# Kernel tuning notes

Hardware: AMD Instinct MI355X
Metric: run time of the kernel (lower is better)

The kernel has to match this reference:

```python
import jax, jax.numpy as jnp
import numpy as np

NUM_HEADS = 8
NUM_GROUPS = 32
EPS = 1e-5


def group_norm(x, gamma, beta):
    B, C, H, W = x.shape
    xg = x.reshape(B, NUM_GROUPS, C // NUM_GROUPS * H * W)
    mean = xg.mean(axis=-1, keepdims=True)
    var = xg.var(axis=-1, keepdims=True)
    xg = (xg - mean) * jax.lax.rsqrt(var + EPS)
    xn = xg.reshape(B, C, H, W)
    return xn * gamma[None, :, None, None] + beta[None, :, None, None]


def setup_inputs() -> dict:
    key = jax.random.key(0)
    ks = jax.random.split(key, 7)
    C = 512
    B, H, W = 8, 32, 32
    x = jax.random.normal(ks[0], (B, C, H, W), dtype=jnp.float32)
    gamma = jnp.ones((C,), dtype=jnp.float32)
    beta = jnp.zeros((C,), dtype=jnp.float32)
    # 1x1 conv weights stored as [out, in]
    w_qkv = jax.random.normal(ks[1], (3 * C, C), dtype=jnp.float32) * (1.0 / np.sqrt(C))
    b_qkv = jax.random.normal(ks[2], (3 * C,), dtype=jnp.float32) * 0.02
    w_proj = jax.random.normal(ks[3], (C, C), dtype=jnp.float32) * (1.0 / np.sqrt(C))
    b_proj = jax.random.normal(ks[4], (C,), dtype=jnp.float32) * 0.02
    return {"x": x, "gamma": gamma, "beta": beta, "w_qkv": w_qkv,
            "b_qkv": b_qkv, "w_proj": w_proj, "b_proj": b_proj}


def reference(x, gamma, beta, w_qkv, b_qkv, w_proj, b_proj):
    B, C, H, W = x.shape
    hd = C // NUM_HEADS  # head_dim
    x_norm = group_norm(x, gamma, beta)
    # 1x1 conv: [B,C,H,W] x [3C,C] -> [B,3C,H,W]
    qkv = jnp.einsum('bchw,oc->bohw', x_norm, w_qkv) + b_qkv[None, :, None, None]
    q, k, v = jnp.split(qkv, 3, axis=1)
    N = H * W
    q = q.reshape(B, NUM_HEADS, hd, N)
    k = k.reshape(B, NUM_HEADS, hd, N)
    v = v.reshape(B, NUM_HEADS, hd, N)
    attn = jnp.einsum('bhcn,bhcm->bhnm', q, k) * (hd ** -0.5)
    attn = jax.nn.softmax(attn, axis=-1)
    out = jnp.einsum('bhnm,bhcm->bhcn', attn, v)
    out = out.reshape(B, C, H, W)
    proj = jnp.einsum('bchw,oc->bohw', out, w_proj) + b_proj[None, :, None, None]
    return x + proj
```

## Files before the change

kernel.cpp:

```cpp
#include <hip/hip_runtime.h>
#include <hip/hip_bf16.h>

#define BB 8
#define CC 512
#define NN 1024
#define NG 32
#define CPG 16
#define NH 8
#define HD 64
#define C3 1536
#define QKLD 1024

typedef __hip_bfloat16 bf16;
typedef unsigned short ushort_t;

typedef __attribute__((ext_vector_type(8))) short bf16x8;
typedef __attribute__((ext_vector_type(8))) unsigned short ushortx8;
typedef __attribute__((ext_vector_type(4))) float floatx4;

__device__ __forceinline__ float b2f(bf16 h) { return __bfloat162float(h); }
__device__ __forceinline__ bf16 f2b(float f) { return __float2bfloat16(f); }
__device__ __forceinline__ float us2f(ushort_t u) {
    union { unsigned int i; float f; } c; c.i = ((unsigned int)u) << 16; return c.f;
}
__device__ __forceinline__ ushort_t f2us(float f) {
    bf16 h = __float2bfloat16(f);
    return *(ushort_t*)&h;
}

__global__ __launch_bounds__(256) void gn_kernel(const float* __restrict__ x,
                                                 const float* __restrict__ gamma,
                                                 const float* __restrict__ beta,
                                                 bf16* __restrict__ xnT,
                                                 const float* __restrict__ wqkv,
                                                 const float* __restrict__ wproj,
                                                 ushort_t* __restrict__ wqkvB,
                                                 ushort_t* __restrict__ wprojB) {
    int tid = threadIdx.x;
    if (blockIdx.x >= 256) {
        int wb = blockIdx.x - 256;
        int base = (wb * 256 + tid) * 4;
        const int STR = 16 * 256 * 4;
        for (int i = base; i < C3 * CC; i += STR) {
            float4 f = *(const float4*)(wqkv + i);
            ushort_t u[4] = {f2us(f.x), f2us(f.y), f2us(f.z), f2us(f.w)};
            *(uint2*)(wqkvB + i) = *(uint2*)u;
        }
        for (int i = base; i < CC * CC; i += STR) {
            float4 f = *(const float4*)(wproj + i);
            ushort_t u[4] = {f2us(f.x), f2us(f.y), f2us(f.z), f2us(f.w)};
            *(uint2*)(wprojB + i) = *(uint2*)u;
        }
        return;
    }

    const int GSZ = CPG * NN;
    int b = blockIdx.x >> 5;
    int g = blockIdx.x & 31;
    size_t base = ((size_t)b * CC + (size_t)g * CPG) * NN;

    int c_loc = tid >> 4;
    int nsp   = (tid & 15) * 16;
    const float* srcrow = x + base + (size_t)c_loc * NN;

    float fv[4][16];
    float s = 0.f, s2 = 0.f;
#pragma unroll
    for (int nc = 0; nc < 4; ++nc) {
        int nb = nc * 256 + nsp;
        *(float4*)(fv[nc] + 0)  = *(const float4*)(srcrow + nb + 0);
        *(float4*)(fv[nc] + 4)  = *(const float4*)(srcrow + nb + 4);
        *(float4*)(fv[nc] + 8)  = *(const float4*)(srcrow + nb + 8);
        *(float4*)(fv[nc] + 12) = *(const float4*)(srcrow + nb + 12);
#pragma unroll
        for (int j = 0; j < 16; ++j) { float v = fv[nc][j]; s += v; s2 += v * v; }
    }

#pragma unroll
    for (int off = 32; off > 0; off >>= 1) {
        s  += __shfl_down(s, off, 64);
        s2 += __shfl_down(s2, off, 64);
    }
    __shared__ float rs[4], rs2[4], stat[2];
    __shared__ ushort_t Lt[16][264];
    int wid = tid >> 6, lane = tid & 63;
    if (lane == 0) { rs[wid] = s; rs2[wid] = s2; }
    __syncthreads();
    if (tid == 0) {
        float ts  = rs[0] + rs[1] + rs[2] + rs[3];
        float ts2 = rs2[0] + rs2[1] + rs2[2] + rs2[3];
        float mean = ts * (1.f / GSZ);
        float var  = ts2 * (1.f / GSZ) - mean * mean;
        stat[0] = mean;
        stat[1] = rsqrtf(var + 1e-5f);
    }
    __syncthreads();
    float mean = stat[0], inv = stat[1];

    float ga = gamma[g * CPG + c_loc];
    float be = beta[g * CPG + c_loc];

    for (int nc = 0; nc < 4; ++nc) {
        ushortx8 u0, u1;
#pragma unroll
        for (int j = 0; j < 8; ++j) {
            u0[j] = f2us((fv[nc][j]     - mean) * inv * ga + be);
            u1[j] = f2us((fv[nc][j + 8] - mean) * inv * ga + be);
        }
        *(ushortx8*)&Lt[c_loc][nsp]     = u0;
        *(ushortx8*)&Lt[c_loc][nsp + 8] = u1;
        __syncthreads();
        ushort_t o16[16];
#pragma unroll
        for (int c = 0; c < 16; ++c) o16[c] = Lt[c][tid];
        ushort_t* dst = (ushort_t*)xnT + ((size_t)b * NN + nc * 256 + tid) * CC + g * CPG;
        *(uint4*)dst       = *(const uint4*)(o16);
        *(uint4*)(dst + 8) = *(const uint4*)(o16 + 8);
        __syncthreads();
    }
}

#define GSTR 40
__global__ __launch_bounds__(256) void qkv_gemm(const ushort_t* __restrict__ wB,
                                                const bf16* __restrict__ xnT,
                                                const float* __restrict__ bias,
                                                bf16* __restrict__ qkT,
                                                bf16* __restrict__ vN) {
    __shared__ ushort_t Wl[128 * GSTR];
    __shared__ ushort_t Xl[128 * GSTR];
    int b  = blockIdx.z;
    int o0 = blockIdx.y * 128;
    int n0 = blockIdx.x * 128;
    int tid = threadIdx.x;
    int wv = tid >> 6, ln = tid & 15, qd = (tid >> 4) & 3;
    int wm = wv >> 1, wn = wv & 1;

    int srow = tid >> 1;
    int kh   = (tid & 1) * 16;
    const ushort_t* wp = wB + (size_t)(o0 + srow) * CC + kh;
    const ushort_t* xp = (const ushort_t*)xnT + ((size_t)b * NN + n0 + srow) * CC + kh;

    floatx4 acc[4][4];
#pragma unroll
    for (int i = 0; i < 4; ++i)
#pragma unroll
        for (int j = 0; j < 4; ++j) acc[i][j] = (floatx4){0.f, 0.f, 0.f, 0.f};

    uint4 wr0, wr1, xr0, xr1;
    wr0 = *(const uint4*)(wp);
    wr1 = *(const uint4*)(wp + 8);
    xr0 = *(const uint4*)(xp);
    xr1 = *(const uint4*)(xp + 8);

    for (int k0 = 0; k0 < CC; k0 += 32) {
        *(uint4*)&Wl[srow * GSTR + kh]     = wr0;
        *(uint4*)&Wl[srow * GSTR + kh + 8] = wr1;
        *(uint4*)&Xl[srow * GSTR + kh]     = xr0;
        *(uint4*)&Xl[srow * GSTR + kh + 8] = xr1;
        __syncthreads();
        if (k0 + 32 < CC) {
            int kn = k0 + 32;
            wr0 = *(const uint4*)(wp + kn);
            wr1 = *(const uint4*)(wp + kn + 8);
            xr0 = *(const uint4*)(xp + kn);
            xr1 = *(const uint4*)(xp + kn + 8);
        }
        bf16x8 af[4], bfr[4];
#pragma unroll
        for (int i = 0; i < 4; ++i)
            af[i] = *(const bf16x8*)&Wl[(wm * 64 + i * 16 + ln) * GSTR + qd * 8];
#pragma unroll
        for (int j = 0; j < 4; ++j)
            bfr[j] = *(const bf16x8*)&Xl[(wn * 64 + j * 16 + ln) * GSTR + qd * 8];
#pragma unroll
        for (int i = 0; i < 4; ++i)
#pragma unroll
            for (int j = 0; j < 4; ++j)
                acc[i][j] = __builtin_amdgcn_mfma_f32_16x16x32_bf16(af[i], bfr[j], acc[i][j], 0, 0, 0);
        __syncthreads();
    }

    if (o0 < 1024) {
#pragma unroll
        for (int i = 0; i < 4; ++i) {
            int ob = o0 + wm * 64 + i * 16 + qd * 4;
            float sc = (ob < 512) ? 0.18033688011112042f : 1.0f;
#pragma unroll
            for (int j = 0; j < 4; ++j) {
                int n = n0 + wn * 64 + j * 16 + ln;
                ushort_t pk[4];
#pragma unroll
                for (int r = 0; r < 4; ++r)
                    pk[r] = f2us((acc[i][j][r] + bias[ob + r]) * sc);
                *(uint2*)((ushort_t*)qkT + ((size_t)b * NN + n) * QKLD + ob) = *(uint2*)pk;
            }
        }
    } else {
#pragma unroll
        for (int i = 0; i < 4; ++i) {
#pragma unroll
            for (int r = 0; r < 4; ++r) {
                int o = o0 + wm * 64 + i * 16 + qd * 4 + r;
                float bb = bias[o];
                size_t rb = ((size_t)b * CC + (o - 1024)) * NN + n0 + wn * 64 + ln;
#pragma unroll
                for (int j = 0; j < 4; ++j)
                    vN[rb + j * 16] = f2b(acc[i][j][r] + bb);
            }
        }
    }
}

__global__ __launch_bounds__(256, 4) void attn_kernel(const bf16* __restrict__ qkTp,
                                                      const bf16* __restrict__ vNp,
                                                      bf16* __restrict__ aoT) {
    __shared__ ushort_t Kt[2][64 * 64];
    __shared__ ushort_t Vn[2][64 * 64];
    __shared__ ushort_t Pw[4][16 * 64];

    int h  = blockIdx.x;
    int qt = blockIdx.y;
    int bi = blockIdx.z;
    int q0 = qt * 64;
    int tid = threadIdx.x;
    int wq = tid >> 6;
    int l  = tid & 63;
    int ln = l & 15;
    int qd = (l >> 4) & 3;
    int l7 = ln & 7;
    int lb = ln >> 3;

    const ushort_t* qkT = (const ushort_t*)qkTp;
    const ushort_t* vN  = (const ushort_t*)vNp;

    const ushort_t* qsrc = qkT + ((size_t)bi * NN + q0 + wq * 16 + ln) * QKLD + h * HD + qd * 8;
    bf16x8 aq0 = *(const bf16x8*)(qsrc);
    bf16x8 aq1 = *(const bf16x8*)(qsrc + 32);

    bf16x8 ones;
#pragma unroll
    for (int j = 0; j < 8; ++j) ones[j] = (short)0x3F80;

    floatx4 O[4];
#pragma unroll
    for (int t = 0; t < 4; ++t) O[t] = (floatx4){0.f, 0.f, 0.f, 0.f};
    floatx4 lsum = (floatx4){0.f, 0.f, 0.f, 0.f};

    ushort_t* Pme = &Pw[wq][0];

    int ksl0 = (qd ^ l7) * 8;
    int ksl1 = ((qd + 4) ^ l7) * 8;

    int srow = tid >> 2;
    int g1   = tid & 3;
    int s7   = srow & 7;
    int ko1  = (g1 ^ s7) * 8;
    int ko2  = ((g1 + 4) ^ s7) * 8;
    const ushort_t* ks = qkT + ((size_t)bi * NN + srow) * QKLD + 512 + h * HD + g1 * 8;
    const ushort_t* vs = vN + ((size_t)bi * CC + h * HD + srow) * NN + g1 * 8;

    uint4 kr0 = *(const uint4*)(ks);
    uint4 kr1 = *(const uint4*)(ks + 32);
    uint4 vr0 = *(const uint4*)(vs);
    uint4 vr1 = *(const uint4*)(vs + 32);
    {
        ushort_t* kd = &Kt[0][srow * 64];
        *(uint4*)(kd + ko1) = kr0; *(uint4*)(kd + ko2) = kr1;
        ushort_t* vd = &Vn[0][srow * 64];
        *(uint4*)(vd + ko1) = vr0; *(uint4*)(vd + ko2) = vr1;
    }
    kr0 = *(const uint4*)(ks + (size_t)64 * QKLD);
    kr1 = *(const uint4*)(ks + (size_t)64 * QKLD + 32);
    vr0 = *(const uint4*)(vs + 64);
    vr1 = *(const uint4*)(vs + 64 + 32);
    __syncthreads();

    for (int it = 0; it < 16; ++it) {
        int cur = it & 1;
        const ushort_t* KtC = &Kt[cur][0];
        const ushort_t* VnC = &Vn[cur][0];
        if (it < 15) {
            ushort_t* kd = &Kt[cur ^ 1][srow * 64];
            *(uint4*)(kd + ko1) = kr0; *(uint4*)(kd + ko2) = kr1;
            ushort_t* vd = &Vn[cur ^ 1][srow * 64];
            *(uint4*)(vd + ko1) = vr0; *(uint4*)(vd + ko2) = vr1;
        }
        if (it < 14) {
            size_t mo = (size_t)(it + 2) * 64;
            kr0 = *(const uint4*)(ks + mo * QKLD);
            kr1 = *(const uint4*)(ks + mo * QKLD + 32);
            vr0 = *(const uint4*)(vs + mo);
            vr1 = *(const uint4*)(vs + mo + 32);
        }

        floatx4 S[4];
#pragma unroll
        for (int t = 0; t < 4; ++t) {
            const ushort_t* krow = KtC + (t * 16 + ln) * 64;
            bf16x8 b0 = *(const bf16x8*)(krow + ksl0);
            bf16x8 b1 = *(const bf16x8*)(krow + ksl1);
            floatx4 acc = (floatx4){0.f, 0.f, 0.f, 0.f};
            acc = __builtin_amdgcn_mfma_f32_16x16x32_bf16(aq0, b0, acc, 0, 0, 0);
            acc = __builtin_amdgcn_mfma_f32_16x16x32_bf16(aq1, b1, acc, 0, 0, 0);
            S[t] = acc;
        }

#pragma unroll
        for (int t = 0; t < 4; ++t) {
#pragma unroll
            for (int r = 0; r < 4; ++r) {
                float p = exp2f(S[t][r]);
                int qr = qd * 4 + r;
                Pme[qr * 64 + ((t * 2 + lb) ^ (qr & 7)) * 8 + l7] = f2us(p);
            }
        }
        bf16x8 pa0 = *(const bf16x8*)&Pme[ln * 64 + ksl0];
        bf16x8 pa1 = *(const bf16x8*)&Pme[ln * 64 + ksl1];

        lsum = __builtin_amdgcn_mfma_f32_16x16x32_bf16(pa0, ones, lsum, 0, 0, 0);
        lsum = __builtin_amdgcn_mfma_f32_16x16x32_bf16(pa1, ones, lsum, 0, 0, 0);

#pragma unroll
        for (int t = 0; t < 4; ++t) {
            const ushort_t* vrow = VnC + (t * 16 + ln) * 64;
            bf16x8 v0 = *(const bf16x8*)(vrow + ksl0);
            bf16x8 v1 = *(const bf16x8*)(vrow + ksl1);
            O[t] = __builtin_amdgcn_mfma_f32_16x16x32_bf16(pa0, v0, O[t], 0, 0, 0);
            O[t] = __builtin_amdgcn_mfma_f32_16x16x32_bf16(pa1, v1, O[t], 0, 0, 0);
        }
        if (it < 15) __syncthreads();
    }

    float inv[4];
#pragma unroll
    for (int r = 0; r < 4; ++r) inv[r] = 1.f / lsum[r];
#pragma unroll
    for (int t = 0; t < 4; ++t) {
#pragma unroll
        for (int r = 0; r < 4; ++r) {
            int n = q0 + wq * 16 + qd * 4 + r;
            ((ushort_t*)aoT)[((size_t)bi * NN + n) * CC + h * HD + t * 16 + ln] =
                f2us(O[t][r] * inv[r]);
        }
    }
}

__global__ __launch_bounds__(256) void proj_gemm(const bf16* __restrict__ aoT,
                                                 const ushort_t* __restrict__ wB,
                                                 const float* __restrict__ bias,
                                                 const float* __restrict__ xres,
                                                 float* __restrict__ out) {
    __shared__ ushort_t Wl[64 * GSTR];
    __shared__ ushort_t Xl[128 * GSTR];
    int b  = blockIdx.z;
    int o0 = blockIdx.y * 64;
    int n0 = blockIdx.x * 128;
    int tid = threadIdx.x;
    int wv = tid >> 6, ln = tid & 15, qd = (tid >> 4) & 3;
    int wm = wv >> 1, wn = wv & 1;

    int srow = tid >> 1;
    int kh   = (tid & 1) * 16;
    const ushort_t* xp = (const ushort_t*)aoT + ((size_t)b * NN + n0 + srow) * CC + kh;
    const ushort_t* wp = wB + (size_t)(o0 + (srow & 63)) * CC + kh;
    bool doW = (tid < 128);

    floatx4 acc[2][4];
#pragma unroll
    for (int i = 0; i < 2; ++i)
#pragma unroll
        for (int j = 0; j < 4; ++j) acc[i][j] = (floatx4){0.f, 0.f, 0.f, 0.f};

    uint4 wr0, wr1, xr0, xr1;
    if (doW) {
        wr0 = *(const uint4*)(wp);
        wr1 = *(const uint4*)(wp + 8);
    }
    xr0 = *(const uint4*)(xp);
    xr1 = *(const uint4*)(xp + 8);

    for (int k0 = 0; k0 < CC; k0 += 32) {
        if (doW) {
            *(uint4*)&Wl[(srow & 63) * GSTR + kh]     = wr0;
            *(uint4*)&Wl[(srow & 63) * GSTR + kh + 8] = wr1;
        }
        *(uint4*)&Xl[srow * GSTR + kh]     = xr0;
        *(uint4*)&Xl[srow * GSTR + kh + 8] = xr1;
        __syncthreads();
        if (k0 + 32 < CC) {
            int kn = k0 + 32;
            if (doW) {
                wr0 = *(const uint4*)(wp + kn);
                wr1 = *(const uint4*)(wp + kn + 8);
            }
            xr0 = *(const uint4*)(xp + kn);
            xr1 = *(const uint4*)(xp + kn + 8);
        }
        bf16x8 af[2], bfr[4];
#pragma unroll
        for (int i = 0; i < 2; ++i)
            af[i] = *(const bf16x8*)&Wl[(wm * 32 + i * 16 + ln) * GSTR + qd * 8];
#pragma unroll
        for (int j = 0; j < 4; ++j)
            bfr[j] = *(const bf16x8*)&Xl[(wn * 64 + j * 16 + ln) * GSTR + qd * 8];
#pragma unroll
        for (int i = 0; i < 2; ++i)
#pragma unroll
            for (int j = 0; j < 4; ++j)
                acc[i][j] = __builtin_amdgcn_mfma_f32_16x16x32_bf16(af[i], bfr[j], acc[i][j], 0, 0, 0);
        __syncthreads();
    }

#pragma unroll
    for (int i = 0; i < 2; ++i) {
#pragma unroll
        for (int r = 0; r < 4; ++r) {
            int o = o0 + wm * 32 + i * 16 + qd * 4 + r;
            float bb = bias[o];
            size_t rb = ((size_t)b * CC + o) * NN + n0 + wn * 64 + ln;
#pragma unroll
            for (int j = 0; j < 4; ++j)
                out[rb + j * 16] = acc[i][j][r] + bb + xres[rb + j * 16];
        }
    }
}

extern "C" void kernel_launch(void* const* d_in, const int* in_sizes, int n_in,
                              void* d_out, int out_size, void* d_ws, size_t ws_size,
                              hipStream_t stream) {
    const float* x      = (const float*)d_in[0];
    const float* gamma  = (const float*)d_in[1];
    const float* beta   = (const float*)d_in[2];
    const float* w_qkv  = (const float*)d_in[3];
    const float* b_qkv  = (const float*)d_in[4];
    const float* w_proj = (const float*)d_in[5];
    const float* b_proj = (const float*)d_in[6];
    float* out = (float*)d_out;

    bf16* xnT = (bf16*)d_ws;
    bf16* qkT = xnT + (size_t)BB * CC * NN;
    bf16* vN  = qkT + (size_t)BB * NN * QKLD;
    ushort_t* wqkvB  = (ushort_t*)(vN + (size_t)BB * CC * NN);
    ushort_t* wprojB = wqkvB + (size_t)C3 * CC;
    bf16* aoT = xnT;

    gn_kernel<<<BB * NG + 16, 256, 0, stream>>>(x, gamma, beta, xnT,
                                                w_qkv, w_proj, wqkvB, wprojB);
    qkv_gemm<<<dim3(NN / 128, C3 / 128, BB), 256, 0, stream>>>(wqkvB, xnT, b_qkv, qkT, vN);
    attn_kernel<<<dim3(NH, NN / 64, BB), 256, 0, stream>>>(qkT, vN, aoT);
    proj_gemm<<<dim3(NN / 128, CC / 64, BB), 256, 0, stream>>>(aoT, wprojB, b_proj, x, out);
}
```

Baseline: 174.7 us.

## Use direct global-to-LDS loads with XOR swizzle in GEMMs and widen weight conversion

Both GEMM kernels now fill shared memory with global_load_lds 16-byte direct transfers instead of staging through registers. Unpadded 32-wide tiles with an XOR swizzle avoid bank conflicts. Register prefetch of the next k-tile is dropped, so global latency is no longer overlapped with MFMA compute, but VGPR use and LDS store instructions go down. The weight bf16 conversion in gn_kernel is also spread over 256 extra blocks instead of 16 to increase parallelism.

```diff
diff --git a/kernel.cpp b/kernel.cpp
--- a/kernel.cpp
+++ b/kernel.cpp
@@ -20,13 +20,15 @@
 
 __device__ __forceinline__ float b2f(bf16 h) { return __bfloat162float(h); }
 __device__ __forceinline__ bf16 f2b(float f) { return __float2bfloat16(f); }
-__device__ __forceinline__ float us2f(ushort_t u) {
-    union { unsigned int i; float f; } c; c.i = ((unsigned int)u) << 16; return c.f;
-}
 __device__ __forceinline__ ushort_t f2us(float f) {
     bf16 h = __float2bfloat16(f);
     return *(ushort_t*)&h;
 }
+
+#define GLD16(gsrc, ldst)                                                        \
+    __builtin_amdgcn_global_load_lds(                                            \
+        (const __attribute__((address_space(1))) unsigned int*)(const void*)(gsrc), \
+        (__attribute__((address_space(3))) unsigned int*)(void*)(ldst), 16, 0, 0)
 
 __global__ __launch_bounds__(256) void gn_kernel(const float* __restrict__ x,
                                                  const float* __restrict__ gamma,
@@ -39,17 +41,17 @@
     int tid = threadIdx.x;
     if (blockIdx.x >= 256) {
         int wb = blockIdx.x - 256;
-        int base = (wb * 256 + tid) * 4;
-        const int STR = 16 * 256 * 4;
-        for (int i = base; i < C3 * CC; i += STR) {
-            float4 f = *(const float4*)(wqkv + i);
+        const float* src;
+        ushort_t* dst;
+        int base;
+        if (wb < 192) { src = wqkv; dst = wqkvB; base = wb * 4096; }
+        else          { src = wproj; dst = wprojB; base = (wb - 192) * 4096; }
+        int o = base + tid * 4;
+#pragma unroll
+        for (int it = 0; it < 4; ++it) {
+            float4 f = *(const float4*)(src + o + it * 1024);
             ushort_t u[4] = {f2us(f.x), f2us(f.y), f2us(f.z), f2us(f.w)};
-            *(uint2*)(wqkvB + i) = *(uint2*)u;
-        }
-        for (int i = base; i < CC * CC; i += STR) {
-            float4 f = *(const float4*)(wproj + i);
-            ushort_t u[4] = {f2us(f.x), f2us(f.y), f2us(f.z), f2us(f.w)};
-            *(uint2*)(wprojB + i) = *(uint2*)u;
+            *(uint2*)(dst + o + it * 1024) = *(uint2*)u;
         }
         return;
     }
@@ -120,25 +122,28 @@
     }
 }
 
-#define GSTR 40
 __global__ __launch_bounds__(256) void qkv_gemm(const ushort_t* __restrict__ wB,
                                                 const bf16* __restrict__ xnT,
                                                 const float* __restrict__ bias,
                                                 bf16* __restrict__ qkT,
                                                 bf16* __restrict__ vN) {
-    __shared__ ushort_t Wl[128 * GSTR];
-    __shared__ ushort_t Xl[128 * GSTR];
+    __shared__ ushort_t Wl[128 * 32];
+    __shared__ ushort_t Xl[128 * 32];
     int b  = blockIdx.z;
     int o0 = blockIdx.y * 128;
     int n0 = blockIdx.x * 128;
     int tid = threadIdx.x;
-    int wv = tid >> 6, ln = tid & 15, qd = (tid >> 4) & 3;
+    int wv = tid >> 6, l = tid & 63, ln = l & 15, qd = (l >> 4) & 3;
     int wm = wv >> 1, wn = wv & 1;
 
-    int srow = tid >> 1;
-    int kh   = (tid & 1) * 16;
-    const ushort_t* wp = wB + (size_t)(o0 + srow) * CC + kh;
-    const ushort_t* xp = (const ushort_t*)xnT + ((size_t)b * NN + n0 + srow) * CC + kh;
+    int strow = wv * 32 + (l >> 2);
+    int sgran = (l & 3) ^ ((l >> 2) & 3);
+    const ushort_t* wsrc = wB + (size_t)(o0 + strow) * CC + sgran * 8;
+    const ushort_t* xsrc = (const ushort_t*)xnT + ((size_t)b * NN + n0 + strow) * CC + sgran * 8;
+    ushort_t* wl0 = &Wl[(wv * 32) * 32];
+    ushort_t* wl1 = &Wl[(wv * 32 + 16) * 32];
+    ushort_t* xl0 = &Xl[(wv * 32) * 32];
+    ushort_t* xl1 = &Xl[(wv * 32 + 16) * 32];
 
     floatx4 acc[4][4];
 #pragma unroll
@@ -146,32 +151,21 @@
 #pragma unroll
         for (int j = 0; j < 4; ++j) acc[i][j] = (floatx4){0.f, 0.f, 0.f, 0.f};
 
-    uint4 wr0, wr1, xr0, xr1;
-    wr0 = *(const uint4*)(wp);
-    wr1 = *(const uint4*)(wp + 8);
-    xr0 = *(const uint4*)(xp);
-    xr1 = *(const uint4*)(xp + 8);
+    int qs = (qd ^ (ln & 3)) * 8;
 
     for (int k0 = 0; k0 < CC; k0 += 32) {
-        *(uint4*)&Wl[srow * GSTR + kh]     = wr0;
-        *(uint4*)&Wl[srow * GSTR + kh + 8] = wr1;
-        *(uint4*)&Xl[srow * GSTR + kh]     = xr0;
-        *(uint4*)&Xl[srow * GSTR + kh + 8] = xr1;
-        __syncthreads();
-        if (k0 + 32 < CC) {
-            int kn = k0 + 32;
-            wr0 = *(const uint4*)(wp + kn);
-            wr1 = *(const uint4*)(wp + kn + 8);
-            xr0 = *(const uint4*)(xp + kn);
-            xr1 = *(const uint4*)(xp + kn + 8);
-        }
+        GLD16(wsrc + k0, wl0);
+        GLD16(wsrc + k0 + 16 * CC, wl1);
+        GLD16(xsrc + k0, xl0);
+        GLD16(xsrc + k0 + 16 * CC, xl1);
+        __syncthreads();
         bf16x8 af[4], bfr[4];
 #pragma unroll
         for (int i = 0; i < 4; ++i)
-            af[i] = *(const bf16x8*)&Wl[(wm * 64 + i * 16 + ln) * GSTR + qd * 8];
+            af[i] = *(const bf16x8*)&Wl[(wm * 64 + i * 16 + ln) * 32 + qs];
 #pragma unroll
         for (int j = 0; j < 4; ++j)
-            bfr[j] = *(const bf16x8*)&Xl[(wn * 64 + j * 16 + ln) * GSTR + qd * 8];
+            bfr[j] = *(const bf16x8*)&Xl[(wn * 64 + j * 16 + ln) * 32 + qs];
 #pragma unroll
         for (int i = 0; i < 4; ++i)
 #pragma unroll
@@ -350,20 +344,23 @@
                                                  const float* __restrict__ bias,
                                                  const float* __restrict__ xres,
                                                  float* __restrict__ out) {
-    __shared__ ushort_t Wl[64 * GSTR];
-    __shared__ ushort_t Xl[128 * GSTR];
+    __shared__ ushort_t Wl[64 * 32];
+    __shared__ ushort_t Xl[128 * 32];
     int b  = blockIdx.z;
     int o0 = blockIdx.y * 64;
     int n0 = blockIdx.x * 128;
     int tid = threadIdx.x;
-    int wv = tid >> 6, ln = tid & 15, qd = (tid >> 4) & 3;
+    int wv = tid >> 6, l = tid & 63, ln = l & 15, qd = (l >> 4) & 3;
     int wm = wv >> 1, wn = wv & 1;
 
-    int srow = tid >> 1;
-    int kh   = (tid & 1) * 16;
-    const ushort_t* xp = (const ushort_t*)aoT + ((size_t)b * NN + n0 + srow) * CC + kh;
-    const ushort_t* wp = wB + (size_t)(o0 + (srow & 63)) * CC + kh;
-    bool doW = (tid < 128);
+    int strow = wv * 32 + (l >> 2);
+    int sgran = (l & 3) ^ ((l >> 2) & 3);
+    const ushort_t* xsrc = (const ushort_t*)aoT + ((size_t)b * NN + n0 + strow) * CC + sgran * 8;
+    int wrow = wv * 16 + (l >> 2);
+    const ushort_t* wsrc = wB + (size_t)(o0 + wrow) * CC + sgran * 8;
+    ushort_t* xl0 = &Xl[(wv * 32) * 32];
+    ushort_t* xl1 = &Xl[(wv * 32 + 16) * 32];
+    ushort_t* wl0 = &Wl[(wv * 16) * 32];
 
     floatx4 acc[2][4];
 #pragma unroll
@@ -371,38 +368,20 @@
 #pragma unroll
         for (int j = 0; j < 4; ++j) acc[i][j] = (floatx4){0.f, 0.f, 0.f, 0.f};
 
-    uint4 wr0, wr1, xr0, xr1;
-    if (doW) {
-        wr0 = *(const uint4*)(wp);
-        wr1 = *(const uint4*)(wp + 8);
-    }
-    xr0 = *(const uint4*)(xp);
-    xr1 = *(const uint4*)(xp + 8);
+    int qs = (qd ^ (ln & 3)) * 8;
 
     for (int k0 = 0; k0 < CC; k0 += 32) {
-        if (doW) {
-            *(uint4*)&Wl[(srow & 63) * GSTR + kh]     = wr0;
-            *(uint4*)&Wl[(srow & 63) * GSTR + kh + 8] = wr1;
-        }
-        *(uint4*)&Xl[srow * GSTR + kh]     = xr0;
-        *(uint4*)&Xl[srow * GSTR + kh + 8] = xr1;
-        __syncthreads();
-        if (k0 + 32 < CC) {
-            int kn = k0 + 32;
-            if (doW) {
-                wr0 = *(const uint4*)(wp + kn);
-                wr1 = *(const uint4*)(wp + kn + 8);
-            }
-            xr0 = *(const uint4*)(xp + kn);
-            xr1 = *(const uint4*)(xp + kn + 8);
-        }
+        GLD16(wsrc + k0, wl0);
+        GLD16(xsrc + k0, xl0);
+        GLD16(xsrc + k0 + 16 * CC, xl1);
+        __syncthreads();
         bf16x8 af[2], bfr[4];
 #pragma unroll
         for (int i = 0; i < 2; ++i)
-            af[i] = *(const bf16x8*)&Wl[(wm * 32 + i * 16 + ln) * GSTR + qd * 8];
+            af[i] = *(const bf16x8*)&Wl[(wm * 32 + i * 16 + ln) * 32 + qs];
 #pragma unroll
         for (int j = 0; j < 4; ++j)
-            bfr[j] = *(const bf16x8*)&Xl[(wn * 64 + j * 16 + ln) * GSTR + qd * 8];
+            bfr[j] = *(const bf16x8*)&Xl[(wn * 64 + j * 16 + ln) * 32 + qs];
 #pragma unroll
         for (int i = 0; i < 2; ++i)
 #pragma unroll
@@ -444,8 +423,8 @@
     ushort_t* wprojB = wqkvB + (size_t)C3 * CC;
     bf16* aoT = xnT;
 
-    gn_kernel<<<BB * NG + 16, 256, 0, stream>>>(x, gamma, beta, xnT,
-                                                w_qkv, w_proj, wqkvB, wprojB);
+    gn_kernel<<<BB * NG + 256, 256, 0, stream>>>(x, gamma, beta, xnT,
+                                                 w_qkv, w_proj, wqkvB, wprojB);
     qkv_gemm<<<dim3(NN / 128, C3 / 128, BB), 256, 0, stream>>>(wqkvB, xnT, b_qkv, qkT, vN);
     attn_kernel<<<dim3(NH, NN / 64, BB), 256, 0, stream>>>(qkT, vN, aoT);
     proj_gemm<<<dim3(NN / 128, CC / 64, BB), 256, 0, stream>>>(aoT, wprojB, b_proj, x, out);
```

After: 163.0 us. -6.7%, faster.
